# Performance work log

Measured on AMD Instinct MI355X. Metric: run time of the kernel, lower is better.

## Reference

```python
import jax, jax.numpy as jnp
import numpy as np

N, D = 8192, 128
TEMPERATURE = 0.07
EPS = 1e-8
NEG_FILL = -9e15


def setup_inputs() -> dict:
    key = jax.random.key(0)
    feats = jax.random.normal(key, (N, D), dtype=jnp.float32)
    # SimCLR-style positive-pair mask: row i's positive is row (i + N//2) % N.
    # Exactly one positive per row, as required by the original broadcast.
    label = jnp.roll(jnp.eye(N, dtype=jnp.int32), N // 2, axis=1)
    return {"feats": feats, "label": label}


def reference(feats, label):
    # F.cosine_similarity clamps each norm at eps before dividing.
    norms = jnp.linalg.norm(feats, axis=-1, keepdims=True)
    nf = feats / jnp.maximum(norms, EPS)            # [N, D] unit rows
    cos_sim = nf @ nf.T                             # [N, N] cosine similarities
    n = cos_sim.shape[0]
    self_mask = jnp.eye(n, dtype=bool)
    cos_sim = jnp.where(self_mask, NEG_FILL, cos_sim)
    cos_sim = cos_sim / TEMPERATURE
    pos_mask = (label == 1)
    # Exactly one positive per row -> masked sum == cos_sim[pos_mask] in row order.
    pos = jnp.sum(jnp.where(pos_mask, cos_sim, 0.0), axis=-1)  # [N]
    lse = jax.nn.logsumexp(cos_sim, axis=-1)                    # [N]
    return jnp.mean(-pos + lse)
```

## Files before the change

kernel.cpp:

```cpp
#include <hip/hip_runtime.h>


#define NN 8192
#define DD 128

typedef __bf16 bf16x8 __attribute__((ext_vector_type(8)));
typedef float f32x4 __attribute__((ext_vector_type(4)));
typedef unsigned int u32x4 __attribute__((ext_vector_type(4)));

constexpr float kM     = 1.0f / 0.07f;
constexpr float kScale = 1.4426950408889634f / 0.07f;
constexpr float kLn2   = 0.6931471805599453f;

__device__ inline unsigned short f2bf(float f) {
  unsigned int u = __float_as_uint(f);
  unsigned int r = (u + 0x7FFFu + ((u >> 16) & 1u)) >> 16;
  return (unsigned short)r;
}

__global__ __launch_bounds__(256) void k_normalize(const float* __restrict__ feats,
                                                   unsigned short* __restrict__ nfb) {
  int tid = threadIdx.x;
  int lane = tid & 63;
  int row = blockIdx.x * 4 + (tid >> 6);
  float2 f = *(const float2*)(feats + (size_t)row * DD + lane * 2);
  float ss = f.x * f.x + f.y * f.y;
  #pragma unroll
  for (int m = 1; m < 64; m <<= 1) ss += __shfl_xor(ss, m);
  float rn = 1.0f / fmaxf(sqrtf(ss), 1e-8f);
  unsigned int lo = f2bf(f.x * rn), hi = f2bf(f.y * rn);
  *(unsigned int*)(nfb + (size_t)row * DD + lane * 2) = lo | (hi << 16);
}

__global__ __launch_bounds__(256) void k_fused(const unsigned short* __restrict__ nfb,
                                               const int* __restrict__ label,
                                               float* __restrict__ lpart,
                                               int* __restrict__ pos_idx) {
  __shared__ __align__(16) unsigned short ldsB[64 * DD];
  int b = blockIdx.x;
  int tid = threadIdx.x;
  if (b & 1) {
    int g = b >> 1;
    int r0 = (g >> 2) * 64;
    int c0 = (g & 3) * 2048;
    int lane = tid & 63, w = tid >> 6;
    int wm = w >> 1, wn = w & 1;
    int lg = lane >> 4;
    int ll = lane & 15;

    bf16x8 afr[2][4];
    #pragma unroll
    for (int ms = 0; ms < 2; ms++) {
      const unsigned short* arow = nfb + (size_t)(r0 + wm * 32 + ms * 16 + ll) * DD + lg * 8;
      #pragma unroll
      for (int kc = 0; kc < 4; kc++)
        afr[ms][kc] = *(const bf16x8*)(arow + kc * 32);
    }

    float lacc[2][4] = {{0.f, 0.f, 0.f, 0.f}, {0.f, 0.f, 0.f, 0.f}};
    int slr = tid >> 4;
    int sch = tid & 15;

    for (int ct = 0; ct < 32; ct++) {
      int ctile = c0 + ct * 64;
      __syncthreads();
      #pragma unroll
      for (int p = 0; p < 4; p++) {
        int row = p * 16 + slr;
        u32x4 v = *(const u32x4*)(nfb + (size_t)(ctile + row) * DD + sch * 8);
        *(u32x4*)((char*)ldsB + row * 256 + ((sch * 16) ^ ((row & 7) << 4))) = v;
      }
      __syncthreads();

      f32x4 acc[2][2] = {{{0.f,0.f,0.f,0.f},{0.f,0.f,0.f,0.f}},
                         {{0.f,0.f,0.f,0.f},{0.f,0.f,0.f,0.f}}};
      #pragma unroll
      for (int ns = 0; ns < 2; ns++) {
        int brow = wn * 32 + ns * 16 + ll;
        const char* bbase = (const char*)ldsB + brow * 256;
        int sw = (brow & 7) << 4;
        #pragma unroll
        for (int kc = 0; kc < 4; kc++) {
          bf16x8 bfr = *(const bf16x8*)(bbase + ((kc * 64 + lg * 16) ^ sw));
          acc[0][ns] = __builtin_amdgcn_mfma_f32_16x16x32_bf16(afr[0][kc], bfr, acc[0][ns], 0, 0, 0);
          acc[1][ns] = __builtin_amdgcn_mfma_f32_16x16x32_bf16(afr[1][kc], bfr, acc[1][ns], 0, 0, 0);
        }
      }

      bool mayDiag = (ctile < r0 + 64) && (r0 < ctile + 64);
      if (mayDiag) {
        #pragma unroll
        for (int ms = 0; ms < 2; ms++) {
          int growb = r0 + wm * 32 + ms * 16 + lg * 4;
          #pragma unroll
          for (int ns = 0; ns < 2; ns++) {
            int gcol = ctile + wn * 32 + ns * 16 + ll;
            #pragma unroll
            for (int r = 0; r < 4; r++) {
              float s = (growb + r == gcol) ? -3.0e38f : acc[ms][ns][r];
              lacc[ms][r] += __builtin_amdgcn_exp2f((s - 1.0f) * kScale);
            }
          }
        }
      } else {
        #pragma unroll
        for (int ms = 0; ms < 2; ms++)
          #pragma unroll
          for (int ns = 0; ns < 2; ns++)
            #pragma unroll
            for (int r = 0; r < 4; r++)
              lacc[ms][r] += __builtin_amdgcn_exp2f((acc[ms][ns][r] - 1.0f) * kScale);
      }
    }

    #pragma unroll
    for (int ms = 0; ms < 2; ms++)
      #pragma unroll
      for (int r = 0; r < 4; r++) {
        float v = lacc[ms][r];
        v += __shfl_xor(v, 1); v += __shfl_xor(v, 2);
        v += __shfl_xor(v, 4); v += __shfl_xor(v, 8);
        lacc[ms][r] = v;
      }
    if (ll == 0) {
      int slot = (g & 3) * 2 + wn;
      #pragma unroll
      for (int ms = 0; ms < 2; ms++)
        #pragma unroll
        for (int r = 0; r < 4; r++) {
          int grow = r0 + wm * 32 + ms * 16 + lg * 4 + r;
          lpart[(size_t)slot * NN + grow] = lacc[ms][r];
        }
    }
  } else {
    int sg = b >> 1;
    const u32x4* L = (const u32x4*)label;
    int t = sg * 256 + tid;
    for (int k = 0; k < 16; k++) {
      u32x4 v[8];
      #pragma unroll
      for (int j = 0; j < 8; j++)
        v[j] = __builtin_nontemporal_load(&L[t + (k * 8 + j) * 131072]);
      unsigned any = 0;
      #pragma unroll
      for (int j = 0; j < 8; j++) any |= v[j][0] | v[j][1] | v[j][2] | v[j][3];
      if (any) {
        #pragma unroll
        for (int j = 0; j < 8; j++) {
          int idx = t + (k * 8 + j) * 131072;
          if (v[j][0] | v[j][1] | v[j][2] | v[j][3]) {
            int gi = idx * 4;
            int row = gi >> 13, col = gi & (NN - 1);
            if (v[j][0] == 1u) pos_idx[row] = col;
            if (v[j][1] == 1u) pos_idx[row] = col + 1;
            if (v[j][2] == 1u) pos_idx[row] = col + 2;
            if (v[j][3] == 1u) pos_idx[row] = col + 3;
          }
        }
      }
    }
  }
}

__global__ __launch_bounds__(256) void k_finalize(const unsigned short* __restrict__ nfb,
                                                  const float* __restrict__ lpart,
                                                  const int* __restrict__ pos_idx,
                                                  float* __restrict__ bpart) {
  int i = blockIdx.x * 256 + threadIdx.x;
  float l = 0.f;
  #pragma unroll
  for (int s = 0; s < 8; s++) l += lpart[(size_t)s * NN + i];
  float lse = kM + __builtin_amdgcn_logf(l) * kLn2;
  int p = pos_idx[i] & (NN - 1);
  const u32x4* ri = (const u32x4*)(nfb + (size_t)i * DD);
  const u32x4* rp = (const u32x4*)(nfb + (size_t)p * DD);
  float dot = 0.f;
  #pragma unroll
  for (int c = 0; c < 16; c++) {
    u32x4 a = ri[c], bb = rp[c];
    #pragma unroll
    for (int e = 0; e < 4; e++) {
      float al = __uint_as_float(a[e] << 16), ah = __uint_as_float(a[e] & 0xFFFF0000u);
      float bl = __uint_as_float(bb[e] << 16), bh = __uint_as_float(bb[e] & 0xFFFF0000u);
      dot += al * bl + ah * bh;
    }
  }
  float val = lse - dot * kM;
  #pragma unroll
  for (int m = 1; m < 64; m <<= 1) val += __shfl_xor(val, m);
  __shared__ float wsum[4];
  if ((threadIdx.x & 63) == 0) wsum[threadIdx.x >> 6] = val;
  __syncthreads();
  if (threadIdx.x == 0) bpart[blockIdx.x] = wsum[0] + wsum[1] + wsum[2] + wsum[3];
}

__global__ void k_reduce(const float* __restrict__ bpart, float* __restrict__ out) {
  int t = threadIdx.x;
  float v = (t < 32) ? bpart[t] : 0.f;
  #pragma unroll
  for (int m = 1; m < 64; m <<= 1) v += __shfl_xor(v, m);
  if (t == 0) out[0] = v * (1.0f / (float)NN);
}

extern "C" void kernel_launch(void* const* d_in, const int* in_sizes, int n_in,
                              void* d_out, int out_size, void* d_ws, size_t ws_size,
                              hipStream_t stream) {
  (void)in_sizes; (void)n_in; (void)out_size; (void)ws_size;
  const float* feats = (const float*)d_in[0];
  const int* label = (const int*)d_in[1];
  float* out = (float*)d_out;

  char* ws = (char*)d_ws;
  unsigned short* nfb = (unsigned short*)ws;
  float* lpart = (float*)(ws + 2 * 1024 * 1024);
  int* pos_idx = (int*)(ws + 2 * 1024 * 1024 + 262144);
  float* bpart = (float*)(ws + 2 * 1024 * 1024 + 262144 + 32768);

  k_normalize<<<NN / 4, 256, 0, stream>>>(feats, nfb);
  k_fused<<<1024, 256, 0, stream>>>(nfb, label, lpart, pos_idx);
  k_finalize<<<NN / 256, 256, 0, stream>>>(nfb, lpart, pos_idx, bpart);
  k_reduce<<<1, 64, 0, stream>>>(bpart, out);
}
```

Measured before the change: 72.20 us.

## Rebalance fused kernel block split between label scan and GEMM-LSE tiles

Reassigns the 1024 blocks of the fused kernel so 640 blocks scan the label matrix with contiguous chunks (regular loads, clamped indices) and 384 blocks loop over the 512 GEMM/logsumexp tiles. It also adds a launch-bounds occupancy hint. The separate reduce kernel is replaced with an atomicAdd into the output after a memset. The goal is to balance the bandwidth-bound label scan against the MFMA work and to drop one launch. The trade-off is uneven GEMM tile counts per block (some blocks do two tiles) and a nondeterministic atomic summation order.

```diff
diff --git a/kernel.cpp b/kernel.cpp
--- a/kernel.cpp
+++ b/kernel.cpp
@@ -32,124 +32,36 @@
   *(unsigned int*)(nfb + (size_t)row * DD + lane * 2) = lo | (hi << 16);
 }
 
-__global__ __launch_bounds__(256) void k_fused(const unsigned short* __restrict__ nfb,
-                                               const int* __restrict__ label,
-                                               float* __restrict__ lpart,
-                                               int* __restrict__ pos_idx) {
+__global__ __launch_bounds__(256, 3) void k_fused(const unsigned short* __restrict__ nfb,
+                                                  const int* __restrict__ label,
+                                                  float* __restrict__ lpart,
+                                                  int* __restrict__ pos_idx) {
   __shared__ __align__(16) unsigned short ldsB[64 * DD];
   int b = blockIdx.x;
   int tid = threadIdx.x;
-  if (b & 1) {
-    int g = b >> 1;
-    int r0 = (g >> 2) * 64;
-    int c0 = (g & 3) * 2048;
-    int lane = tid & 63, w = tid >> 6;
-    int wm = w >> 1, wn = w & 1;
-    int lg = lane >> 4;
-    int ll = lane & 15;
-
-    bf16x8 afr[2][4];
-    #pragma unroll
-    for (int ms = 0; ms < 2; ms++) {
-      const unsigned short* arow = nfb + (size_t)(r0 + wm * 32 + ms * 16 + ll) * DD + lg * 8;
-      #pragma unroll
-      for (int kc = 0; kc < 4; kc++)
-        afr[ms][kc] = *(const bf16x8*)(arow + kc * 32);
-    }
-
-    float lacc[2][4] = {{0.f, 0.f, 0.f, 0.f}, {0.f, 0.f, 0.f, 0.f}};
-    int slr = tid >> 4;
-    int sch = tid & 15;
-
-    for (int ct = 0; ct < 32; ct++) {
-      int ctile = c0 + ct * 64;
-      __syncthreads();
-      #pragma unroll
-      for (int p = 0; p < 4; p++) {
-        int row = p * 16 + slr;
-        u32x4 v = *(const u32x4*)(nfb + (size_t)(ctile + row) * DD + sch * 8);
-        *(u32x4*)((char*)ldsB + row * 256 + ((sch * 16) ^ ((row & 7) << 4))) = v;
-      }
-      __syncthreads();
-
-      f32x4 acc[2][2] = {{{0.f,0.f,0.f,0.f},{0.f,0.f,0.f,0.f}},
-                         {{0.f,0.f,0.f,0.f},{0.f,0.f,0.f,0.f}}};
-      #pragma unroll
-      for (int ns = 0; ns < 2; ns++) {
-        int brow = wn * 32 + ns * 16 + ll;
-        const char* bbase = (const char*)ldsB + brow * 256;
-        int sw = (brow & 7) << 4;
-        #pragma unroll
-        for (int kc = 0; kc < 4; kc++) {
-          bf16x8 bfr = *(const bf16x8*)(bbase + ((kc * 64 + lg * 16) ^ sw));
-          acc[0][ns] = __builtin_amdgcn_mfma_f32_16x16x32_bf16(afr[0][kc], bfr, acc[0][ns], 0, 0, 0);
-          acc[1][ns] = __builtin_amdgcn_mfma_f32_16x16x32_bf16(afr[1][kc], bfr, acc[1][ns], 0, 0, 0);
-        }
-      }
-
-      bool mayDiag = (ctile < r0 + 64) && (r0 < ctile + 64);
-      if (mayDiag) {
-        #pragma unroll
-        for (int ms = 0; ms < 2; ms++) {
-          int growb = r0 + wm * 32 + ms * 16 + lg * 4;
-          #pragma unroll
-          for (int ns = 0; ns < 2; ns++) {
-            int gcol = ctile + wn * 32 + ns * 16 + ll;
-            #pragma unroll
-            for (int r = 0; r < 4; r++) {
-              float s = (growb + r == gcol) ? -3.0e38f : acc[ms][ns][r];
-              lacc[ms][r] += __builtin_amdgcn_exp2f((s - 1.0f) * kScale);
-            }
-          }
-        }
-      } else {
-        #pragma unroll
-        for (int ms = 0; ms < 2; ms++)
-          #pragma unroll
-          for (int ns = 0; ns < 2; ns++)
-            #pragma unroll
-            for (int r = 0; r < 4; r++)
-              lacc[ms][r] += __builtin_amdgcn_exp2f((acc[ms][ns][r] - 1.0f) * kScale);
-      }
-    }
-
-    #pragma unroll
-    for (int ms = 0; ms < 2; ms++)
-      #pragma unroll
-      for (int r = 0; r < 4; r++) {
-        float v = lacc[ms][r];
-        v += __shfl_xor(v, 1); v += __shfl_xor(v, 2);
-        v += __shfl_xor(v, 4); v += __shfl_xor(v, 8);
-        lacc[ms][r] = v;
-      }
-    if (ll == 0) {
-      int slot = (g & 3) * 2 + wn;
-      #pragma unroll
-      for (int ms = 0; ms < 2; ms++)
-        #pragma unroll
-        for (int r = 0; r < 4; r++) {
-          int grow = r0 + wm * 32 + ms * 16 + lg * 4 + r;
-          lpart[(size_t)slot * NN + grow] = lacc[ms][r];
-        }
-    }
-  } else {
-    int sg = b >> 1;
+  int c = b & 255;
+  if (c < 160) {
+    int s = (b >> 8) * 160 + c;
     const u32x4* L = (const u32x4*)label;
-    int t = sg * 256 + tid;
-    for (int k = 0; k < 16; k++) {
+    int base = s * 26624 + tid;
+    for (int bb = 0; bb < 13; ++bb) {
       u32x4 v[8];
       #pragma unroll
-      for (int j = 0; j < 8; j++)
-        v[j] = __builtin_nontemporal_load(&L[t + (k * 8 + j) * 131072]);
+      for (int j = 0; j < 8; j++) {
+        unsigned idx = (unsigned)(base + bb * 2048 + j * 256);
+        idx = idx < 16777216u ? idx : 16777215u;
+        v[j] = L[idx];
+      }
       unsigned any = 0;
       #pragma unroll
       for (int j = 0; j < 8; j++) any |= v[j][0] | v[j][1] | v[j][2] | v[j][3];
       if (any) {
         #pragma unroll
         for (int j = 0; j < 8; j++) {
-          int idx = t + (k * 8 + j) * 131072;
           if (v[j][0] | v[j][1] | v[j][2] | v[j][3]) {
-            int gi = idx * 4;
+            unsigned idx = (unsigned)(base + bb * 2048 + j * 256);
+            idx = idx < 16777216u ? idx : 16777215u;
+            int gi = (int)idx * 4;
             int row = gi >> 13, col = gi & (NN - 1);
             if (v[j][0] == 1u) pos_idx[row] = col;
             if (v[j][1] == 1u) pos_idx[row] = col + 1;
@@ -159,13 +71,109 @@
         }
       }
     }
+  } else {
+    int p = (b >> 8) * 96 + (c - 160);
+    int lane = tid & 63, w = tid >> 6;
+    int wm = w >> 1, wn = w & 1;
+    int lg = lane >> 4;
+    int ll = lane & 15;
+    int slr = tid >> 4;
+    int sch = tid & 15;
+
+    for (int u = p; u < 512; u += 384) {
+      int r0 = (u >> 2) * 64;
+      int c0 = (u & 3) * 2048;
+
+      bf16x8 afr[2][4];
+      #pragma unroll
+      for (int ms = 0; ms < 2; ms++) {
+        const unsigned short* arow = nfb + (size_t)(r0 + wm * 32 + ms * 16 + ll) * DD + lg * 8;
+        #pragma unroll
+        for (int kc = 0; kc < 4; kc++)
+          afr[ms][kc] = *(const bf16x8*)(arow + kc * 32);
+      }
+
+      float lacc[2][4] = {{0.f, 0.f, 0.f, 0.f}, {0.f, 0.f, 0.f, 0.f}};
+
+      for (int ct = 0; ct < 32; ct++) {
+        int ctile = c0 + ct * 64;
+        __syncthreads();
+        #pragma unroll
+        for (int pp = 0; pp < 4; pp++) {
+          int row = pp * 16 + slr;
+          u32x4 v = *(const u32x4*)(nfb + (size_t)(ctile + row) * DD + sch * 8);
+          *(u32x4*)((char*)ldsB + row * 256 + ((sch * 16) ^ ((row & 7) << 4))) = v;
+        }
+        __syncthreads();
+
+        f32x4 acc[2][2] = {{{0.f,0.f,0.f,0.f},{0.f,0.f,0.f,0.f}},
+                           {{0.f,0.f,0.f,0.f},{0.f,0.f,0.f,0.f}}};
+        #pragma unroll
+        for (int ns = 0; ns < 2; ns++) {
+          int brow = wn * 32 + ns * 16 + ll;
+          const char* bbase = (const char*)ldsB + brow * 256;
+          int sw = (brow & 7) << 4;
+          #pragma unroll
+          for (int kc = 0; kc < 4; kc++) {
+            bf16x8 bfr = *(const bf16x8*)(bbase + ((kc * 64 + lg * 16) ^ sw));
+            acc[0][ns] = __builtin_amdgcn_mfma_f32_16x16x32_bf16(afr[0][kc], bfr, acc[0][ns], 0, 0, 0);
+            acc[1][ns] = __builtin_amdgcn_mfma_f32_16x16x32_bf16(afr[1][kc], bfr, acc[1][ns], 0, 0, 0);
+          }
+        }
+
+        bool mayDiag = (ctile < r0 + 64) && (r0 < ctile + 64);
+        if (mayDiag) {
+          #pragma unroll
+          for (int ms = 0; ms < 2; ms++) {
+            int growb = r0 + wm * 32 + ms * 16 + lg * 4;
+            #pragma unroll
+            for (int ns = 0; ns < 2; ns++) {
+              int gcol = ctile + wn * 32 + ns * 16 + ll;
+              #pragma unroll
+              for (int r = 0; r < 4; r++) {
+                float sv = (growb + r == gcol) ? -3.0e38f : acc[ms][ns][r];
+                lacc[ms][r] += __builtin_amdgcn_exp2f((sv - 1.0f) * kScale);
+              }
+            }
+          }
+        } else {
+          #pragma unroll
+          for (int ms = 0; ms < 2; ms++)
+            #pragma unroll
+            for (int ns = 0; ns < 2; ns++)
+              #pragma unroll
+              for (int r = 0; r < 4; r++)
+                lacc[ms][r] += __builtin_amdgcn_exp2f((acc[ms][ns][r] - 1.0f) * kScale);
+        }
+      }
+
+      #pragma unroll
+      for (int ms = 0; ms < 2; ms++)
+        #pragma unroll
+        for (int r = 0; r < 4; r++) {
+          float v = lacc[ms][r];
+          v += __shfl_xor(v, 1); v += __shfl_xor(v, 2);
+          v += __shfl_xor(v, 4); v += __shfl_xor(v, 8);
+          lacc[ms][r] = v;
+        }
+      if (ll == 0) {
+        int slot = (u & 3) * 2 + wn;
+        #pragma unroll
+        for (int ms = 0; ms < 2; ms++)
+          #pragma unroll
+          for (int r = 0; r < 4; r++) {
+            int grow = r0 + wm * 32 + ms * 16 + lg * 4 + r;
+            lpart[(size_t)slot * NN + grow] = lacc[ms][r];
+          }
+      }
+    }
   }
 }
 
 __global__ __launch_bounds__(256) void k_finalize(const unsigned short* __restrict__ nfb,
                                                   const float* __restrict__ lpart,
                                                   const int* __restrict__ pos_idx,
-                                                  float* __restrict__ bpart) {
+                                                  float* __restrict__ out) {
   int i = blockIdx.x * 256 + threadIdx.x;
   float l = 0.f;
   #pragma unroll
@@ -191,15 +199,8 @@
   __shared__ float wsum[4];
   if ((threadIdx.x & 63) == 0) wsum[threadIdx.x >> 6] = val;
   __syncthreads();
-  if (threadIdx.x == 0) bpart[blockIdx.x] = wsum[0] + wsum[1] + wsum[2] + wsum[3];
-}
-
-__global__ void k_reduce(const float* __restrict__ bpart, float* __restrict__ out) {
-  int t = threadIdx.x;
-  float v = (t < 32) ? bpart[t] : 0.f;
-  #pragma unroll
-  for (int m = 1; m < 64; m <<= 1) v += __shfl_xor(v, m);
-  if (t == 0) out[0] = v * (1.0f / (float)NN);
+  if (threadIdx.x == 0)
+    atomicAdd(out, (wsum[0] + wsum[1] + wsum[2] + wsum[3]) * (1.0f / (float)NN));
 }
 
 extern "C" void kernel_launch(void* const* d_in, const int* in_sizes, int n_in,
@@ -214,10 +215,9 @@
   unsigned short* nfb = (unsigned short*)ws;
   float* lpart = (float*)(ws + 2 * 1024 * 1024);
   int* pos_idx = (int*)(ws + 2 * 1024 * 1024 + 262144);
-  float* bpart = (float*)(ws + 2 * 1024 * 1024 + 262144 + 32768);
-
+
+  hipMemsetAsync(out, 0, sizeof(float), stream);
   k_normalize<<<NN / 4, 256, 0, stream>>>(feats, nfb);
   k_fused<<<1024, 256, 0, stream>>>(nfb, label, lpart, pos_idx);
-  k_finalize<<<NN / 256, 256, 0, stream>>>(nfb, lpart, pos_idx, bpart);
-  k_reduce<<<1, 64, 0, stream>>>(bpart, out);
-}
+  k_finalize<<<NN / 256, 256, 0, stream>>>(nfb, lpart, pos_idx, out);
+}
```

Result: slower. 88.30 us (+22.3%).
